# Performance work log

Measured on AMD Instinct MI355X. Metric: run time of the kernel, lower is better.

## Reference

```python
import jax, jax.numpy as jnp
import numpy as np

R, E, N, B = 64, 100000, 1000000, 4

def setup_inputs() -> dict:
    key = jax.random.key(0)
    k1, k2, k3 = jax.random.split(key, 3)
    p = jax.random.normal(k1, (R,), dtype=jnp.float32)
    edges = jax.random.randint(k2, (R, E, 2), 0, N, dtype=jnp.int64)
    x = jax.random.normal(k3, (B, N), dtype=jnp.float32)
    return {"p": p, "edges": edges, "x": x}

def reference(p, edges, x):
    # _A = sum_r p[r] * (A_r + A_r^T), with A_r[u,v] += 1 per edge (duplicates sum,
    # matching scipy csr_matrix construction). y = x @ _A, i.e.
    # y[b, j] = sum over edges (u,v) of relation r: p[r]*x[b,u] into j=v and p[r]*x[b,v] into j=u.
    num_entities = x.shape[1]
    e = edges.shape[1]
    src = edges[..., 0].reshape(-1)            # [R*E]
    dst = edges[..., 1].reshape(-1)            # [R*E]
    w = jnp.repeat(p, e)                       # [R*E] per-edge relation weight
    # include inverse edges
    srcs = jnp.concatenate([src, dst])         # [2RE]
    dsts = jnp.concatenate([dst, src])         # [2RE]
    ww = jnp.concatenate([w, w])               # [2RE]
    vals = x[:, srcs].T * ww[:, None]          # [2RE, B] gathered & weighted messages
    y = jax.ops.segment_sum(vals, dsts, num_segments=num_entities).T  # [B, N]
    return y
```

## Files before the change

### kernel.cpp

```cpp
#include <hip/hip_runtime.h>
#include <hip/hip_fp16.h>


constexpr int  R_   = 64;
constexpr long E_   = 100000;
constexpr int  N_   = 1000000;
constexpr long RE_  = (long)R_ * E_;
constexpr long M2_  = 2 * RE_;
constexpr int  BSH  = 11;
constexpr int  BUCKET = 1 << BSH;
constexpr int  NB   = (N_ + BUCKET - 1) >> BSH;
constexpr int  NBP  = 512;
constexpr int  EPB  = 4096;
constexpr int  HB   = (int)((RE_ + EPB - 1) / EPB);
constexpr int  RPB  = 2 * EPB;
constexpr int  MCH  = 8192;
constexpr int  MBB  = (int)((M2_ + MCH - 1) / MCH);

__global__ __launch_bounds__(256) void k_transpose_h(const float* __restrict__ x,
                                                     uint2* __restrict__ xTh) {
    int i = blockIdx.x * 256 + threadIdx.x;
    if (i < N_) {
        __half2 a = __floats2half2_rn(x[i],           x[(long)N_ + i]);
        __half2 b = __floats2half2_rn(x[2L * N_ + i], x[3L * N_ + i]);
        xTh[i] = make_uint2(__builtin_bit_cast(unsigned, a),
                            __builtin_bit_cast(unsigned, b));
    }
}

__global__ __launch_bounds__(256) void k_hist(const unsigned long long* __restrict__ edges8,
                                              int* __restrict__ g_bcnt) {
    __shared__ int lc[NB];
    for (int i = threadIdx.x; i < NB; i += 256) lc[i] = 0;
    __syncthreads();
    long k0 = (long)blockIdx.x * EPB;
    int lim = (int)min((long)EPB, RE_ - k0);
    for (int i = threadIdx.x; i < lim; i += 256) {
        unsigned long long ev = __builtin_nontemporal_load(edges8 + k0 + i);
        unsigned u = (unsigned)ev, v = (unsigned)(ev >> 32);
        atomicAdd(&lc[u >> BSH], 1);
        atomicAdd(&lc[v >> BSH], 1);
    }
    __syncthreads();
    for (int c = threadIdx.x; c < NB; c += 256)
        g_bcnt[(size_t)c * HB + blockIdx.x] = lc[c];
}

__global__ __launch_bounds__(256) void k_colsum(const int* __restrict__ g_bcnt,
                                                int* __restrict__ ctot) {
    __shared__ int red[256];
    const int c = blockIdx.x, t = threadIdx.x;
    int s = 0;
    for (int b = t; b < HB; b += 256) s += g_bcnt[(size_t)c * HB + b];
    red[t] = s;
    __syncthreads();
    for (int off = 128; off > 0; off >>= 1) {
        if (t < off) red[t] += red[t + off];
        __syncthreads();
    }
    if (t == 0) ctot[c] = red[0];
}

__global__ __launch_bounds__(512) void k_scan(const int* __restrict__ ctot,
                                              int* __restrict__ cbase,
                                              int* __restrict__ tailA,
                                              int* __restrict__ tailB) {
    __shared__ int sA[NBP], sB[NBP];
    int t = threadIdx.x;
    sA[t] = (t < NB) ? ctot[t] : 0;
    __syncthreads();
    int* A = sA; int* B = sB;
    for (int off = 1; off < NBP; off <<= 1) {
        int v = A[t];
        if (t >= off) v += A[t - off];
        B[t] = v;
        __syncthreads();
        int* tmp = A; A = B; B = tmp;
    }
    if (t < NB) { int e = t ? A[t - 1] : 0; cbase[t] = e; tailA[t] = e; tailB[t] = e; }
    if (t == 0) cbase[NB] = A[NB - 1];
}

__global__ __launch_bounds__(1024) void k_srcbin(const unsigned long long* __restrict__ edges8,
                                                 const int* __restrict__ g_bcnt,
                                                 int* __restrict__ g_tailA,
                                                 unsigned short* __restrict__ g_sl,
                                                 unsigned* __restrict__ g_dr) {
    __shared__ unsigned l_src[RPB];
    __shared__ unsigned l_dr[RPB];
    __shared__ int sA[NBP], sB[NBP];
    __shared__ int excl[NB], cur[NB], slab[NB];
    const int t = threadIdx.x, blk = blockIdx.x;
    if (t < NBP) sA[t] = (t < NB) ? g_bcnt[(size_t)t * HB + blk] : 0;
    __syncthreads();
    int* A = sA; int* B = sB;
    for (int off = 1; off < NBP; off <<= 1) {
        if (t < NBP) { int v = A[t]; if (t >= off) v += A[t - off]; B[t] = v; }
        __syncthreads();
        int* tmp = A; A = B; B = tmp;
    }
    if (t < NB) { int e = t ? A[t - 1] : 0; excl[t] = e; cur[t] = e; }
    __syncthreads();

    const long k0 = (long)blk * EPB;
    const int lim = (int)min((long)EPB, RE_ - k0);
    const unsigned r0 = (unsigned)(k0 / E_);
    const long bnd = (long)(r0 + 1) * E_;
    #pragma unroll
    for (int j = 0; j < EPB / 1024; ++j) {
        int i = t + j * 1024;
        if (i < lim) {
            unsigned long long ev = __builtin_nontemporal_load(edges8 + k0 + i);
            unsigned u = (unsigned)ev, v = (unsigned)(ev >> 32);
            unsigned r = (k0 + i >= bnd) ? r0 + 1 : r0;
            int p1 = atomicAdd(&cur[u >> BSH], 1);
            l_src[p1] = u;
            l_dr[p1]  = v | (r << 20);
            int p2 = atomicAdd(&cur[v >> BSH], 1);
            l_src[p2] = v;
            l_dr[p2]  = u | (r << 20);
        }
    }
    __syncthreads();
    for (int c = t; c < NB; c += 1024) {
        int cnt = cur[c] - excl[c];
        slab[c] = cnt ? atomicAdd(&g_tailA[c], cnt) : 0;
    }
    __syncthreads();
    const int total = 2 * lim;
    for (int s = t; s < total; s += 1024) {
        unsigned src = l_src[s];
        int c = (int)(src >> BSH);
        int pos = slab[c] + (s - excl[c]);
        g_sl[pos] = (unsigned short)(src & (BUCKET - 1));
        __builtin_nontemporal_store(l_dr[s], g_dr + pos);
    }
}

__global__ __launch_bounds__(1024) void k_msgbuild(const unsigned* __restrict__ g_dr,
                                                   const unsigned short* __restrict__ g_sl,
                                                   const int* __restrict__ cbase,
                                                   int* __restrict__ g_tailB,
                                                   const float* __restrict__ p,
                                                   const uint2* __restrict__ xTh,
                                                   unsigned short* __restrict__ g_dst2,
                                                   unsigned long long* __restrict__ g_pay2) {
    __shared__ unsigned l_dst[MCH];
    __shared__ unsigned long long l_pay[MCH];
    __shared__ int sA[NBP], sB[NBP];
    __shared__ int excl[NB], cur[NB], slab[NB];
    __shared__ int cbl[NBP];
    __shared__ float pl[R_];
    const int t = threadIdx.x, blk = blockIdx.x;
    if (t < R_) pl[t] = p[t];
    if (t < NBP) { sA[t] = 0; cbl[t] = (t <= NB) ? cbase[t] : 0x7fffffff; }
    __syncthreads();

    const long m0 = (long)blk * MCH;
    const int lim = (int)min((long)MCH, M2_ - m0);
    unsigned mdr[MCH / 1024];
    unsigned msrc[MCH / 1024];
    #pragma unroll
    for (int j = 0; j < MCH / 1024; ++j) {
        int k = t + j * 1024;
        mdr[j] = 0; msrc[j] = 0;
        if (k < lim) {
            int m = (int)(m0 + k);
            unsigned dr = __builtin_nontemporal_load(g_dr + m);
            unsigned short sl = g_sl[m];
            int lo = 0, hi = NB - 1;
            while (lo < hi) { int mid = (lo + hi + 1) >> 1; if (cbl[mid] <= m) lo = mid; else hi = mid - 1; }
            msrc[j] = ((unsigned)lo << BSH) | sl;
            mdr[j] = dr;
            atomicAdd(&sA[(dr & 0xFFFFFu) >> BSH], 1);
        }
    }
    __syncthreads();
    int* A = sA; int* B = sB;
    for (int off = 1; off < NBP; off <<= 1) {
        if (t < NBP) { int v = A[t]; if (t >= off) v += A[t - off]; B[t] = v; }
        __syncthreads();
        int* tmp = A; A = B; B = tmp;
    }
    if (t < NB) { int e = t ? A[t - 1] : 0; excl[t] = e; cur[t] = e; }
    __syncthreads();
    uint2 xg[MCH / 1024];
    #pragma unroll
    for (int j = 0; j < MCH / 1024; ++j) {
        int k = t + j * 1024;
        if (k < lim) xg[j] = xTh[msrc[j]];
    }
    #pragma unroll
    for (int j = 0; j < MCH / 1024; ++j) {
        int k = t + j * 1024;
        if (k < lim) {
            unsigned dr = mdr[j];
            float w = pl[dr >> 20];
            __half2 h0 = __builtin_bit_cast(__half2, xg[j].x);
            __half2 h1 = __builtin_bit_cast(__half2, xg[j].y);
            unsigned plo = __builtin_bit_cast(unsigned,
                __floats2half2_rn(w * __low2float(h0), w * __high2float(h0)));
            unsigned phi = __builtin_bit_cast(unsigned,
                __floats2half2_rn(w * __low2float(h1), w * __high2float(h1)));
            unsigned dst = dr & 0xFFFFFu;
            int pos = atomicAdd(&cur[dst >> BSH], 1);
            l_dst[pos] = dst;
            l_pay[pos] = ((unsigned long long)phi << 32) | plo;
        }
    }
    __syncthreads();
    for (int c = t; c < NB; c += 1024) {
        int cnt = cur[c] - excl[c];
        slab[c] = cnt ? atomicAdd(&g_tailB[c], cnt) : 0;
    }
    __syncthreads();
    for (int s = t; s < lim; s += 1024) {
        unsigned dst = l_dst[s];
        int c = (int)(dst >> BSH);
        int pos = slab[c] + (s - excl[c]);
        g_dst2[pos] = (unsigned short)(dst & (BUCKET - 1));
        __builtin_nontemporal_store(l_pay[s], g_pay2 + pos);
    }
}

__global__ __launch_bounds__(1024) void k_accum(const unsigned short* __restrict__ g_dst,
                                                const unsigned long long* __restrict__ g_pay,
                                                const int* __restrict__ cbase,
                                                float* __restrict__ y) {
    __shared__ unsigned long long accA[BUCKET];
    __shared__ unsigned long long accB[BUCKET];
    const int t = threadIdx.x, b = blockIdx.x;
    for (int i = t; i < BUCKET; i += 1024) { accA[i] = 0ull; accB[i] = 0ull; }
    __syncthreads();
    const int lo = cbase[b], hi = cbase[b + 1];
    for (int i = lo + t; i < hi; i += 1024) {
        int dl = (int)g_dst[i];
        unsigned long long pay = __builtin_nontemporal_load(g_pay + i);
        __half2 h01 = __builtin_bit_cast(__half2, (unsigned)pay);
        __half2 h23 = __builtin_bit_cast(__half2, (unsigned)(pay >> 32));
        float f0 = fminf(fmaxf(__low2float(h01),  -31.f), 31.f);
        float f1 = fminf(fmaxf(__high2float(h01), -31.f), 31.f);
        float f2 = fminf(fmaxf(__low2float(h23),  -31.f), 31.f);
        float f3 = fminf(fmaxf(__high2float(h23), -31.f), 31.f);
        unsigned e0 = (unsigned)(__float2int_rn(f0 * 65536.f) + (1 << 21));
        unsigned e1 = (unsigned)(__float2int_rn(f1 * 65536.f) + (1 << 21));
        unsigned e2 = (unsigned)(__float2int_rn(f2 * 65536.f) + (1 << 21));
        unsigned e3 = (unsigned)(__float2int_rn(f3 * 65536.f) + (1 << 21));
        unsigned long long va = (unsigned long long)e0
                              | ((unsigned long long)e1 << 28)
                              | (1ull << 56);
        unsigned long long vb = (unsigned long long)e2
                              | ((unsigned long long)e3 << 28);
        atomicAdd(&accA[dl], va);
        atomicAdd(&accB[dl], vb);
    }
    __syncthreads();
    const int base_e = b << BSH;
    for (int j = t; j < BUCKET; j += 1024) {
        int i = base_e + j;
        if (i < N_) {
            unsigned long long a = accA[j], bb = accB[j];
            long deg  = (long)(a >> 56);
            long bias = deg << 21;
            long c0 = (long)(a & 0xFFFFFFFull) - bias;
            long c1 = (long)((a >> 28) & 0xFFFFFFFull) - bias;
            long c2 = (long)(bb & 0xFFFFFFFull) - bias;
            long c3 = (long)((bb >> 28) & 0xFFFFFFFull) - bias;
            const float sc = 1.f / 65536.f;
            y[i]            = (float)c0 * sc;
            y[(long)N_ + i] = (float)c1 * sc;
            y[2L * N_ + i]  = (float)c2 * sc;
            y[3L * N_ + i]  = (float)c3 * sc;
        }
    }
}

__global__ __launch_bounds__(256) void k_scatter_direct(const int2* __restrict__ edges,
                                                        const float* __restrict__ p,
                                                        const float* __restrict__ x,
                                                        float* __restrict__ y) {
    const long stride = (long)gridDim.x * blockDim.x;
    for (long k = (long)blockIdx.x * blockDim.x + threadIdx.x; k < RE_; k += stride) {
        int2 e = edges[k];
        float w = p[(int)(k / E_)];
        #pragma unroll
        for (int b = 0; b < 4; ++b) {
            float xu = x[(long)b * N_ + e.x];
            float xv = x[(long)b * N_ + e.y];
            atomicAdd(&y[(long)b * N_ + e.y], w * xu);
            atomicAdd(&y[(long)b * N_ + e.x], w * xv);
        }
    }
}

extern "C" void kernel_launch(void* const* d_in, const int* in_sizes, int n_in,
                              void* d_out, int out_size, void* d_ws, size_t ws_size,
                              hipStream_t stream) {
    const float* p     = (const float*)d_in[0];
    const int*   edges = (const int*)d_in[1];
    const float* x     = (const float*)d_in[2];
    float*       y     = (float*)d_out;

    const size_t pay_bytes   = (size_t)M2_ * 8;
    const size_t dr_bytes    = (size_t)M2_ * 4;
    const size_t xTh_bytes   = (size_t)N_ * 8;
    const size_t bcnt_bytes  = (size_t)NB * HB * 4;
    const size_t ctot_bytes  = (size_t)NBP * 4;
    const size_t cbase_bytes = (size_t)(NB + 1) * 4;
    const size_t tail_bytes  = (size_t)NB * 4;
    const size_t sl_bytes    = (size_t)M2_ * 2;
    const size_t dst2_bytes  = (size_t)M2_ * 2;
    const size_t need = pay_bytes + dr_bytes + xTh_bytes + bcnt_bytes + ctot_bytes
                      + cbase_bytes + 2 * tail_bytes + sl_bytes + dst2_bytes + 64;

    if (ws_size >= need) {
        char* ws = (char*)d_ws;
        unsigned long long* g_pay2 = (unsigned long long*)ws;  ws += pay_bytes;
        unsigned* g_dr = (unsigned*)ws;               ws += dr_bytes;
        uint2*    xTh  = (uint2*)ws;                  ws += xTh_bytes;
        int* g_bcnt = (int*)ws;                       ws += bcnt_bytes;
        int* ctot   = (int*)ws;                       ws += ctot_bytes;
        int* cbase  = (int*)ws;                       ws += cbase_bytes;
        int* tailA  = (int*)ws;                       ws += tail_bytes;
        int* tailB  = (int*)ws;                       ws += tail_bytes;
        unsigned short* g_sl   = (unsigned short*)ws; ws += sl_bytes;
        unsigned short* g_dst2 = (unsigned short*)ws;

        k_transpose_h<<<(N_ + 255) / 256, 256, 0, stream>>>(x, xTh);
        k_hist<<<HB, 256, 0, stream>>>((const unsigned long long*)edges, g_bcnt);
        k_colsum<<<NB, 256, 0, stream>>>(g_bcnt, ctot);
        k_scan<<<1, 512, 0, stream>>>(ctot, cbase, tailA, tailB);
        k_srcbin<<<HB, 1024, 0, stream>>>((const unsigned long long*)edges, g_bcnt,
                                          tailA, g_sl, g_dr);
        k_msgbuild<<<MBB, 1024, 0, stream>>>((const unsigned*)g_dr,
                                             (const unsigned short*)g_sl,
                                             cbase, tailB, p, (const uint2*)xTh,
                                             g_dst2, g_pay2);
        k_accum<<<NB, 1024, 0, stream>>>((const unsigned short*)g_dst2,
                                         (const unsigned long long*)g_pay2, cbase, y);
    } else {
        hipMemsetAsync(y, 0, (size_t)out_size * sizeof(float), stream);
        k_scatter_direct<<<8192, 256, 0, stream>>>((const int2*)edges, p, x, y);
    }
}
```

Baseline: 283.3 us.

## Coarsen source binning to 16K-entity chunks with local block histogram

```diff
diff --git a/kernel.cpp b/kernel.cpp
--- a/kernel.cpp
+++ b/kernel.cpp
@@ -11,10 +11,12 @@
 constexpr int  BUCKET = 1 << BSH;
 constexpr int  NB   = (N_ + BUCKET - 1) >> BSH;
 constexpr int  NBP  = 512;
+constexpr int  CSH  = 14;
+constexpr int  NC   = ((N_ - 1) >> CSH) + 1;
 constexpr int  EPB  = 4096;
 constexpr int  HB   = (int)((RE_ + EPB - 1) / EPB);
 constexpr int  RPB  = 2 * EPB;
-constexpr int  MCH  = 8192;
+constexpr int  MCH  = 4096;
 constexpr int  MBB  = (int)((M2_ + MCH - 1) / MCH);
 
 __global__ __launch_bounds__(256) void k_transpose_h(const float* __restrict__ x,
@@ -77,62 +79,78 @@
         __syncthreads();
         int* tmp = A; A = B; B = tmp;
     }
-    if (t < NB) { int e = t ? A[t - 1] : 0; cbase[t] = e; tailA[t] = e; tailB[t] = e; }
+    if (t < NB) { int e = t ? A[t - 1] : 0; cbase[t] = e; tailB[t] = e; }
     if (t == 0) cbase[NB] = A[NB - 1];
+    if (t < NC) {
+        int f = t * 8;
+        tailA[t] = f ? A[f - 1] : 0;
+    }
 }
 
 __global__ __launch_bounds__(1024) void k_srcbin(const unsigned long long* __restrict__ edges8,
-                                                 const int* __restrict__ g_bcnt,
                                                  int* __restrict__ g_tailA,
                                                  unsigned short* __restrict__ g_sl,
                                                  unsigned* __restrict__ g_dr) {
     __shared__ unsigned l_src[RPB];
     __shared__ unsigned l_dr[RPB];
-    __shared__ int sA[NBP], sB[NBP];
-    __shared__ int excl[NB], cur[NB], slab[NB];
+    __shared__ int sA[64], sB[64];
+    __shared__ int excl[64], cur[64], slab[64];
     const int t = threadIdx.x, blk = blockIdx.x;
-    if (t < NBP) sA[t] = (t < NB) ? g_bcnt[(size_t)t * HB + blk] : 0;
-    __syncthreads();
-    int* A = sA; int* B = sB;
-    for (int off = 1; off < NBP; off <<= 1) {
-        if (t < NBP) { int v = A[t]; if (t >= off) v += A[t - off]; B[t] = v; }
-        __syncthreads();
-        int* tmp = A; A = B; B = tmp;
-    }
-    if (t < NB) { int e = t ? A[t - 1] : 0; excl[t] = e; cur[t] = e; }
+    if (t < 64) sA[t] = 0;
     __syncthreads();
 
     const long k0 = (long)blk * EPB;
     const int lim = (int)min((long)EPB, RE_ - k0);
-    const unsigned r0 = (unsigned)(k0 / E_);
-    const long bnd = (long)(r0 + 1) * E_;
     #pragma unroll
     for (int j = 0; j < EPB / 1024; ++j) {
         int i = t + j * 1024;
         if (i < lim) {
             unsigned long long ev = __builtin_nontemporal_load(edges8 + k0 + i);
             unsigned u = (unsigned)ev, v = (unsigned)(ev >> 32);
+            atomicAdd(&sA[u >> CSH], 1);
+            atomicAdd(&sA[v >> CSH], 1);
+        }
+    }
+    __syncthreads();
+    {
+        int* A = sA; int* B = sB;
+        for (int off = 1; off < 64; off <<= 1) {
+            if (t < 64) { int v = A[t]; if (t >= off) v += A[t - off]; B[t] = v; }
+            __syncthreads();
+            int* tmp = A; A = B; B = tmp;
+        }
+        if (t < 64) { int e = t ? A[t - 1] : 0; excl[t] = e; cur[t] = e; }
+    }
+    __syncthreads();
+    const unsigned r0 = (unsigned)(k0 / E_);
+    const long bnd = (long)(r0 + 1) * E_;
+    #pragma unroll
+    for (int j = 0; j < EPB / 1024; ++j) {
+        int i = t + j * 1024;
+        if (i < lim) {
+            unsigned long long ev = edges8[k0 + i];
+            unsigned u = (unsigned)ev, v = (unsigned)(ev >> 32);
             unsigned r = (k0 + i >= bnd) ? r0 + 1 : r0;
-            int p1 = atomicAdd(&cur[u >> BSH], 1);
+            int p1 = atomicAdd(&cur[u >> CSH], 1);
             l_src[p1] = u;
             l_dr[p1]  = v | (r << 20);
-            int p2 = atomicAdd(&cur[v >> BSH], 1);
+            int p2 = atomicAdd(&cur[v >> CSH], 1);
             l_src[p2] = v;
             l_dr[p2]  = u | (r << 20);
         }
     }
     __syncthreads();
-    for (int c = t; c < NB; c += 1024) {
-        int cnt = cur[c] - excl[c];
-        slab[c] = cnt ? atomicAdd(&g_tailA[c], cnt) : 0;
+    if (t < NC) {
+        int cnt = cur[t] - excl[t];
+        slab[t] = cnt ? atomicAdd(&g_tailA[t], cnt) : 0;
     }
     __syncthreads();
     const int total = 2 * lim;
     for (int s = t; s < total; s += 1024) {
         unsigned src = l_src[s];
-        int c = (int)(src >> BSH);
+        int c = (int)(src >> CSH);
         int pos = slab[c] + (s - excl[c]);
-        g_sl[pos] = (unsigned short)(src & (BUCKET - 1));
+        g_sl[pos] = (unsigned short)(src & ((1u << CSH) - 1));
         __builtin_nontemporal_store(l_dr[s], g_dr + pos);
     }
 }
@@ -149,17 +167,27 @@
     __shared__ unsigned long long l_pay[MCH];
     __shared__ int sA[NBP], sB[NBP];
     __shared__ int excl[NB], cur[NB], slab[NB];
-    __shared__ int cbl[NBP];
+    __shared__ int cbl[NC + 1];
     __shared__ float pl[R_];
+    __shared__ int s_cc0;
     const int t = threadIdx.x, blk = blockIdx.x;
     if (t < R_) pl[t] = p[t];
-    if (t < NBP) { sA[t] = 0; cbl[t] = (t <= NB) ? cbase[t] : 0x7fffffff; }
+    if (t < NBP) sA[t] = 0;
+    if (t <= NC) cbl[t] = cbase[min(t * 8, NB)];
     __syncthreads();
 
     const long m0 = (long)blk * MCH;
     const int lim = (int)min((long)MCH, M2_ - m0);
+    if (t == 0) {
+        int cc = 0;
+        while (cc < NC - 1 && cbl[cc + 1] <= (int)m0) ++cc;
+        s_cc0 = cc;
+    }
+    __syncthreads();
+
     unsigned mdr[MCH / 1024];
     unsigned msrc[MCH / 1024];
+    int cc = s_cc0;
     #pragma unroll
     for (int j = 0; j < MCH / 1024; ++j) {
         int k = t + j * 1024;
@@ -168,21 +196,22 @@
             int m = (int)(m0 + k);
             unsigned dr = __builtin_nontemporal_load(g_dr + m);
             unsigned short sl = g_sl[m];
-            int lo = 0, hi = NB - 1;
-            while (lo < hi) { int mid = (lo + hi + 1) >> 1; if (cbl[mid] <= m) lo = mid; else hi = mid - 1; }
-            msrc[j] = ((unsigned)lo << BSH) | sl;
+            while (cc < NC - 1 && cbl[cc + 1] <= m) ++cc;
+            msrc[j] = ((unsigned)cc << CSH) | sl;
             mdr[j] = dr;
             atomicAdd(&sA[(dr & 0xFFFFFu) >> BSH], 1);
         }
     }
     __syncthreads();
-    int* A = sA; int* B = sB;
-    for (int off = 1; off < NBP; off <<= 1) {
-        if (t < NBP) { int v = A[t]; if (t >= off) v += A[t - off]; B[t] = v; }
-        __syncthreads();
-        int* tmp = A; A = B; B = tmp;
-    }
-    if (t < NB) { int e = t ? A[t - 1] : 0; excl[t] = e; cur[t] = e; }
+    {
+        int* A = sA; int* B = sB;
+        for (int off = 1; off < NBP; off <<= 1) {
+            if (t < NBP) { int v = A[t]; if (t >= off) v += A[t - off]; B[t] = v; }
+            __syncthreads();
+            int* tmp = A; A = B; B = tmp;
+        }
+        if (t < NB) { int e = t ? A[t - 1] : 0; excl[t] = e; cur[t] = e; }
+    }
     __syncthreads();
     uint2 xg[MCH / 1024];
     #pragma unroll
@@ -307,11 +336,13 @@
     const size_t bcnt_bytes  = (size_t)NB * HB * 4;
     const size_t ctot_bytes  = (size_t)NBP * 4;
     const size_t cbase_bytes = (size_t)(NB + 1) * 4;
-    const size_t tail_bytes  = (size_t)NB * 4;
+    const size_t tailA_bytes = (size_t)64 * 4;
+    const size_t tailB_bytes = (size_t)NB * 4;
     const size_t sl_bytes    = (size_t)M2_ * 2;
     const size_t dst2_bytes  = (size_t)M2_ * 2;
     const size_t need = pay_bytes + dr_bytes + xTh_bytes + bcnt_bytes + ctot_bytes
-                      + cbase_bytes + 2 * tail_bytes + sl_bytes + dst2_bytes + 64;
+                      + cbase_bytes + tailA_bytes + tailB_bytes + sl_bytes
+                      + dst2_bytes + 64;
 
     if (ws_size >= need) {
         char* ws = (char*)d_ws;
@@ -321,8 +352,8 @@
         int* g_bcnt = (int*)ws;                       ws += bcnt_bytes;
         int* ctot   = (int*)ws;                       ws += ctot_bytes;
         int* cbase  = (int*)ws;                       ws += cbase_bytes;
-        int* tailA  = (int*)ws;                       ws += tail_bytes;
-        int* tailB  = (int*)ws;                       ws += tail_bytes;
+        int* tailA  = (int*)ws;                       ws += tailA_bytes;
+        int* tailB  = (int*)ws;                       ws += tailB_bytes;
         unsigned short* g_sl   = (unsigned short*)ws; ws += sl_bytes;
         unsigned short* g_dst2 = (unsigned short*)ws;
 
@@ -330,7 +361,7 @@
         k_hist<<<HB, 256, 0, stream>>>((const unsigned long long*)edges, g_bcnt);
         k_colsum<<<NB, 256, 0, stream>>>(g_bcnt, ctot);
         k_scan<<<1, 512, 0, stream>>>(ctot, cbase, tailA, tailB);
-        k_srcbin<<<HB, 1024, 0, stream>>>((const unsigned long long*)edges, g_bcnt,
+        k_srcbin<<<HB, 1024, 0, stream>>>((const unsigned long long*)edges,
                                           tailA, g_sl, g_dr);
         k_msgbuild<<<MBB, 1024, 0, stream>>>((const unsigned*)g_dr,
                                              (const unsigned short*)g_sl,
```

Result: faster. 268.5 us (-5.2%).
